# Optimization experiments

Measured on AMD Instinct MI355X. Metric: run time of the kernel, lower is better.

## Reference

```python
import jax, jax.numpy as jnp
import numpy as np

D_MODEL = 512
N_HEADS = 4  # d_model >= 8 -> 4 heads
HEAD_DIM = D_MODEL // N_HEADS
D_FF = 4 * D_MODEL


def setup_inputs() -> dict:
    key = jax.random.key(0)
    ks = jax.random.split(key, 8)
    B, T = 4, 2048
    s = 0.02
    return {
        "x": jax.random.normal(ks[0], (B, T, D_MODEL), dtype=jnp.float32),
        "ln1_g": jnp.ones((D_MODEL,), jnp.float32),
        "ln1_b": jnp.zeros((D_MODEL,), jnp.float32),
        "w_qkv": jax.random.normal(ks[1], (D_MODEL, 3 * D_MODEL), jnp.float32) * s,
        "w_proj": jax.random.normal(ks[2], (D_MODEL, D_MODEL), jnp.float32) * s,
        "ln2_g": jnp.ones((D_MODEL,), jnp.float32),
        "ln2_b": jnp.zeros((D_MODEL,), jnp.float32),
        "w_ff1": jax.random.normal(ks[3], (D_MODEL, D_FF), jnp.float32) * s,
        "w_ff2": jax.random.normal(ks[4], (D_FF, D_MODEL), jnp.float32) * s,
    }


def _layernorm(x, g, b, eps=1e-5):
    mu = jnp.mean(x, axis=-1, keepdims=True)
    var = jnp.var(x, axis=-1, keepdims=True)
    return (x - mu) * jax.lax.rsqrt(var + eps) * g + b


def _attention(x, w_qkv, w_proj):
    B, T, C = x.shape
    qkv = x @ w_qkv  # [B,T,3C]
    q, k, v = jnp.split(qkv, 3, axis=-1)
    # [B,H,T,Dh]
    q = q.reshape(B, T, N_HEADS, HEAD_DIM).transpose(0, 2, 1, 3)
    k = k.reshape(B, T, N_HEADS, HEAD_DIM).transpose(0, 2, 1, 3)
    v = v.reshape(B, T, N_HEADS, HEAD_DIM).transpose(0, 2, 1, 3)
    scale = 1.0 / jnp.sqrt(jnp.asarray(HEAD_DIM, x.dtype))
    scores = jnp.einsum("bhqd,bhkd->bhqk", q, k) * scale
    causal = jnp.tril(jnp.ones((T, T), bool))
    scores = jnp.where(causal, scores, -jnp.inf)
    attn = jax.nn.softmax(scores, axis=-1)
    out = jnp.einsum("bhqk,bhkd->bhqd", attn, v)
    out = out.transpose(0, 2, 1, 3).reshape(B, T, C)
    return out @ w_proj


def reference(x, ln1_g, ln1_b, w_qkv, w_proj, ln2_g, ln2_b, w_ff1, w_ff2):
    x = x + _attention(_layernorm(x, ln1_g, ln1_b), w_qkv, w_proj)
    h = _layernorm(x, ln2_g, ln2_b)
    h = jax.nn.gelu(h @ w_ff1, approximate=False) @ w_ff2
    return x + h
```

## Files before the change

### kernel.cpp

```cpp
#include <hip/hip_runtime.h>
#include <cstdint>

typedef unsigned short u16;
typedef __attribute__((ext_vector_type(8))) short short8;
typedef __attribute__((ext_vector_type(4))) float floatx4;

#define BT    8192
#define TSEQ  2048
#define NBAT  4
#define CMOD  512
#define NH    4
#define HD    128
#define DFF   2048
#define CQKV  1536

__device__ __forceinline__ u16 f2bf(float f) {
  union { float f; uint32_t u; } v; v.f = f;
  uint32_t r = v.u + 0x7FFFu + ((v.u >> 16) & 1u);
  return (u16)(r >> 16);
}
__device__ __forceinline__ float bf2f(u16 u) {
  union { uint32_t u; float f; } v; v.u = ((uint32_t)u) << 16; return v.f;
}
__device__ __forceinline__ float exp2a(float x) {
  float r; asm("v_exp_f32 %0, %1" : "=v"(r) : "v"(x)); return r;
}
__device__ __forceinline__ float rcpa(float x) {
  float r; asm("v_rcp_f32 %0, %1" : "=v"(r) : "v"(x)); return r;
}

typedef __attribute__((address_space(1))) const unsigned int ga_u32;
typedef __attribute__((address_space(3))) unsigned int ls_u32;
__device__ __forceinline__ void glds16(const u16* g, u16* l) {
  __builtin_amdgcn_global_load_lds((ga_u32*)g, (ls_u32*)l, 16, 0, 0);
}

__device__ __forceinline__ void tcast_body(const float* __restrict__ W, u16* __restrict__ Wt,
                                           int K, int N, int bx, int by, int tid,
                                           float (*tile)[33]) {
  int n0 = bx * 32, k0 = by * 32;
  int tx = tid & 31, ty = tid >> 5;
  #pragma unroll
  for (int r = 0; r < 32; r += 8)
    tile[r + ty][tx] = W[(size_t)(k0 + r + ty) * N + n0 + tx];
  __syncthreads();
  #pragma unroll
  for (int r = 0; r < 32; r += 8)
    Wt[(size_t)(n0 + r + ty) * K + k0 + tx] = f2bf(tile[tx][r + ty]);
}

__global__ __launch_bounds__(256) void prep_kernel(
    const float* __restrict__ x, const float* __restrict__ g, const float* __restrict__ b,
    const float* __restrict__ wqkv, const float* __restrict__ wproj,
    const float* __restrict__ wff1, const float* __restrict__ wff2,
    u16* __restrict__ ln_out, u16* __restrict__ wqkvT, u16* __restrict__ wprojT,
    u16* __restrict__ wff1T, u16* __restrict__ wff2T) {
  __shared__ float tile[32][33];
  int bid = blockIdx.x, tid = threadIdx.x;
  if (bid < 768) {
    tcast_body(wqkv, wqkvT, CMOD, CQKV, bid % 48, bid / 48, tid, tile);
  } else if (bid < 1024) {
    int id = bid - 768; tcast_body(wproj, wprojT, CMOD, CMOD, id % 16, id / 16, tid, tile);
  } else if (bid < 2048) {
    int id = bid - 1024; tcast_body(wff1, wff1T, CMOD, DFF, id % 64, id / 64, tid, tile);
  } else if (bid < 3072) {
    int id = bid - 2048; tcast_body(wff2, wff2T, DFF, CMOD, id % 16, id / 16, tid, tile);
  } else {
    int row = (bid - 3072) * 4 + (tid >> 6);
    int lane = tid & 63;
    const float4* xr = (const float4*)(x + (size_t)row * CMOD);
    float4 a = xr[lane], c = xr[lane + 64];
    float s = a.x + a.y + a.z + a.w + c.x + c.y + c.z + c.w;
    float q = a.x*a.x + a.y*a.y + a.z*a.z + a.w*a.w
            + c.x*c.x + c.y*c.y + c.z*c.z + c.w*c.w;
    #pragma unroll
    for (int o = 32; o; o >>= 1) { s += __shfl_xor(s, o); q += __shfl_xor(q, o); }
    float mu = s * (1.0f / CMOD);
    float rstd = rsqrtf(q * (1.0f / CMOD) - mu * mu + 1e-5f);
    const float4* gr = (const float4*)g;
    const float4* br = (const float4*)b;
    float4 g0 = gr[lane], g1 = gr[lane + 64], b0 = br[lane], b1 = br[lane + 64];
    u16* orow = ln_out + (size_t)row * CMOD;
    int i0 = lane * 4, i1 = (lane + 64) * 4;
    orow[i0 + 0] = f2bf((a.x - mu) * rstd * g0.x + b0.x);
    orow[i0 + 1] = f2bf((a.y - mu) * rstd * g0.y + b0.y);
    orow[i0 + 2] = f2bf((a.z - mu) * rstd * g0.z + b0.z);
    orow[i0 + 3] = f2bf((a.w - mu) * rstd * g0.w + b0.w);
    orow[i1 + 0] = f2bf((c.x - mu) * rstd * g1.x + b1.x);
    orow[i1 + 1] = f2bf((c.y - mu) * rstd * g1.y + b1.y);
    orow[i1 + 2] = f2bf((c.z - mu) * rstd * g1.z + b1.z);
    orow[i1 + 3] = f2bf((c.w - mu) * rstd * g1.w + b1.w);
  }
}

__global__ __launch_bounds__(256) void ln_kernel(const float* __restrict__ x,
                                                 const float* __restrict__ g,
                                                 const float* __restrict__ b,
                                                 u16* __restrict__ out) {
  int row = blockIdx.x * 4 + (threadIdx.x >> 6);
  int lane = threadIdx.x & 63;
  const float4* xr = (const float4*)(x + (size_t)row * CMOD);
  float4 a = xr[lane], c = xr[lane + 64];
  float s = a.x + a.y + a.z + a.w + c.x + c.y + c.z + c.w;
  float q = a.x*a.x + a.y*a.y + a.z*a.z + a.w*a.w
          + c.x*c.x + c.y*c.y + c.z*c.z + c.w*c.w;
  #pragma unroll
  for (int o = 32; o; o >>= 1) { s += __shfl_xor(s, o); q += __shfl_xor(q, o); }
  float mu = s * (1.0f / CMOD);
  float rstd = rsqrtf(q * (1.0f / CMOD) - mu * mu + 1e-5f);
  const float4* gr = (const float4*)g;
  const float4* br = (const float4*)b;
  float4 g0 = gr[lane], g1 = gr[lane + 64], b0 = br[lane], b1 = br[lane + 64];
  u16* orow = out + (size_t)row * CMOD;
  int i0 = lane * 4, i1 = (lane + 64) * 4;
  orow[i0 + 0] = f2bf((a.x - mu) * rstd * g0.x + b0.x);
  orow[i0 + 1] = f2bf((a.y - mu) * rstd * g0.y + b0.y);
  orow[i0 + 2] = f2bf((a.z - mu) * rstd * g0.z + b0.z);
  orow[i0 + 3] = f2bf((a.w - mu) * rstd * g0.w + b0.w);
  orow[i1 + 0] = f2bf((c.x - mu) * rstd * g1.x + b1.x);
  orow[i1 + 1] = f2bf((c.y - mu) * rstd * g1.y + b1.y);
  orow[i1 + 2] = f2bf((c.z - mu) * rstd * g1.z + b1.z);
  orow[i1 + 3] = f2bf((c.w - mu) * rstd * g1.w + b1.w);
}

template <int EPI, int TM, int TN, int MINW>
__global__ __launch_bounds__(256, MINW) void gemm_kernel(
    const u16* __restrict__ A, const u16* __restrict__ Bt, int K,
    const float* __restrict__ resid, float* __restrict__ outf,
    u16* __restrict__ ob0, u16* __restrict__ ob1, u16* __restrict__ ob2) {
  constexpr int MR  = TM / 32;
  constexpr int NR  = TN / 32;
  constexpr int NAR = TM / 64;
  constexpr int NBR = TN / 64;
  __shared__ __align__(16) u16 As[2][TM * 32];
  __shared__ __align__(16) u16 Bs[2][TN * 32];
  int tid = threadIdx.x;
  int lane = tid & 63, wave = tid >> 6;
  int lane16 = lane & 15, quad = lane >> 4;
  int m0 = blockIdx.y * TM, n0 = blockIdx.x * TN;
  int wm = (wave >> 1) * (TM / 2), wn = (wave & 1) * (TN / 2);

  floatx4 acc[MR][NR];
  #pragma unroll
  for (int i = 0; i < MR; i++)
    #pragma unroll
    for (int j = 0; j < NR; j++) acc[i][j] = (floatx4)(0.0f);

  const u16* agp[NAR]; u16* alp[NAR][2];
  const u16* bgp[NBR]; u16* blp[NBR][2];
  #pragma unroll
  for (int i = 0; i < NAR; i++) {
    int s = i * 256 + tid;
    agp[i] = A + (size_t)(m0 + (s >> 2)) * K + (s & 3) * 8;
    alp[i][0] = &As[0][(i * 256 + wave * 64) * 8];
    alp[i][1] = &As[1][(i * 256 + wave * 64) * 8];
  }
  #pragma unroll
  for (int i = 0; i < NBR; i++) {
    int s = i * 256 + tid;
    bgp[i] = Bt + (size_t)(n0 + (s >> 2)) * K + (s & 3) * 8;
    blp[i][0] = &Bs[0][(i * 256 + wave * 64) * 8];
    blp[i][1] = &Bs[1][(i * 256 + wave * 64) * 8];
  }

  int nk = K >> 5;
  #pragma unroll
  for (int i = 0; i < NAR; i++) glds16(agp[i], alp[i][0]);
  #pragma unroll
  for (int i = 0; i < NBR; i++) glds16(bgp[i], blp[i][0]);

  for (int kt = 0; kt < nk; kt++) {
    __syncthreads();
    int buf = kt & 1;
    if (kt + 1 < nk) {
      int k1 = (kt + 1) * 32;
      #pragma unroll
      for (int i = 0; i < NAR; i++) glds16(agp[i] + k1, alp[i][buf ^ 1]);
      #pragma unroll
      for (int i = 0; i < NBR; i++) glds16(bgp[i] + k1, blp[i][buf ^ 1]);
    }
    short8 af[MR];
    #pragma unroll
    for (int i = 0; i < MR; i++)
      af[i] = *(const short8*)&As[buf][(wm + i * 16 + lane16) * 32 + quad * 8];
    #pragma unroll
    for (int j = 0; j < NR; j++) {
      short8 bfj = *(const short8*)&Bs[buf][(wn + j * 16 + lane16) * 32 + quad * 8];
      #pragma unroll
      for (int i = 0; i < MR; i++)
        acc[i][j] = __builtin_amdgcn_mfma_f32_16x16x32_bf16(af[i], bfj, acc[i][j], 0, 0, 0);
    }
  }

  #pragma unroll
  for (int i = 0; i < MR; i++) {
    #pragma unroll
    for (int j = 0; j < NR; j++) {
      #pragma unroll
      for (int r = 0; r < 4; r++) {
        int m = m0 + wm + i * 16 + quad * 4 + r;
        int n = n0 + wn + j * 16 + lane16;
        float v = acc[i][j][r];
        if (EPI == 0) {
          int bb = m >> 11, t = m & 2047;
          int nn = n & 511, which = n >> 9;
          int h = nn >> 7, d = nn & 127;
          size_t base = (size_t)(bb * NH + h) * 262144;
          if (which == 0) {
            int t16 = t >> 4, l16 = t & 15, cc = d >> 5, qd = (d >> 3) & 3, e = d & 7;
            ob0[base + (size_t)((t16 * 16 + cc * 4 + qd) * 128 + l16 * 8 + e)] = f2bf(v * 0.12751743f);
          } else if (which == 1) {
            int kt = t >> 5, hf = (t >> 4) & 1, l16 = t & 15, cc = d >> 5, qd = (d >> 3) & 3, e = d & 7;
            ob1[base + (size_t)((kt * 8 + hf * 4 + cc) * 512 + qd * 128 + l16 * 8 + e)] = f2bf(v);
          } else {
            int kt = t >> 5, qv = (t >> 3) & 3, e = t & 7, j2 = d >> 4, l16 = d & 15;
            ob2[base + (size_t)((kt * 8 + j2) * 512 + qv * 128 + l16 * 8 + e)] = f2bf(v);
          }
        } else if (EPI == 1) {
          size_t idx = (size_t)m * CMOD + n;
          outf[idx] = v + resid[idx];
        } else if (EPI == 2) {
          float ge = 0.5f * v * (1.0f + erff(v * 0.70710678118654752f));
          ob0[(size_t)m * DFF + n] = f2bf(ge);
        } else {
          size_t idx = (size_t)m * CMOD + n;
          outf[idx] = v + resid[idx];
        }
      }
    }
  }
}

__global__ __launch_bounds__(256) void attn_kernel(const u16* __restrict__ qb,
                                                   const u16* __restrict__ kb,
                                                   const u16* __restrict__ vtb,
                                                   u16* __restrict__ po,
                                                   float* __restrict__ pl) {
  int tid = threadIdx.x, wave = tid >> 6, lane = tid & 63;
  int lane16 = lane & 15, quad = lane >> 4;
  int n1d = blockIdx.x;
  int bh = n1d & 15;
  int idx = 143 - (n1d >> 4);
  int g = 1;
  #pragma unroll
  for (int t = 2; t <= 8; t++) if (idx >= 2 * t * (t - 1)) g = t;
  int rem = idx - 2 * g * (g - 1);
  int qi = rem / g;
  int c  = rem - qi * g;
  int qt = ((g - 1) << 2) + qi;

  int q0w = qt * 64 + wave * 16;
  const u16* Qb = qb  + (size_t)bh * 262144;
  const u16* Kb = kb  + (size_t)bh * 262144;
  const u16* Vb = vtb + (size_t)bh * 262144;

  short8 aq[4];
  #pragma unroll
  for (int cc = 0; cc < 4; cc++)
    aq[cc] = *(const short8*)&Qb[(size_t)(((q0w >> 4) * 16 + cc * 4 + quad) * 128 + lane16 * 8)];

  int ktw   = (q0w >> 5) + 1;
  int ktblk = qt * 2 + 2;
  int kt0   = c * 8;
  int kend  = min(min(kt0 + 8, ktblk), ktw);

  floatx4 o[8];
  #pragma unroll
  for (int j = 0; j < 8; j++) o[j] = (floatx4)(0.0f);
  floatx4 ol = (floatx4)(0.0f);

  short8 ones;
  #pragma unroll
  for (int e = 0; e < 8; e++) ones[e] = (short)0x3F80;

  int addrA = (lane16 + ((quad & 1) << 5)) << 2;
  int addrB = addrA + 64;
  int q_g = q0w + lane16;

#define ATTN_TAIL(S0, S1, V_, KT)                                                                   \
  {                                                                                                 \
    int k0b = (KT) * 32 + quad * 4;                                                                 \
    _Pragma("unroll")                                                                               \
    for (int r = 0; r < 4; r++) {                                                                   \
      float p0 = exp2a(S0[r]);                                                                      \
      float p1 = exp2a(S1[r]);                                                                      \
      if (k0b + r > q_g) p0 = 0.0f;                                                                 \
      if (k0b + r + 16 > q_g) p1 = 0.0f;                                                            \
      S0[r] = p0; S1[r] = p1;                                                                       \
    }                                                                                               \
    uint32_t x0 = __builtin_amdgcn_perm(__float_as_uint(S0[1]), __float_as_uint(S0[0]), 0x07060302u); \
    uint32_t x1 = __builtin_amdgcn_perm(__float_as_uint(S0[3]), __float_as_uint(S0[2]), 0x07060302u); \
    uint32_t y0 = __builtin_amdgcn_perm(__float_as_uint(S1[1]), __float_as_uint(S1[0]), 0x07060302u); \
    uint32_t y1 = __builtin_amdgcn_perm(__float_as_uint(S1[3]), __float_as_uint(S1[2]), 0x07060302u); \
    int pAx0 = __builtin_amdgcn_ds_bpermute(addrA, (int)x0);                                        \
    int pAx1 = __builtin_amdgcn_ds_bpermute(addrA, (int)x1);                                        \
    int pBx0 = __builtin_amdgcn_ds_bpermute(addrB, (int)x0);                                        \
    int pBx1 = __builtin_amdgcn_ds_bpermute(addrB, (int)x1);                                        \
    int pAy0 = __builtin_amdgcn_ds_bpermute(addrA, (int)y0);                                        \
    int pAy1 = __builtin_amdgcn_ds_bpermute(addrA, (int)y1);                                        \
    int pBy0 = __builtin_amdgcn_ds_bpermute(addrB, (int)y0);                                        \
    int pBy1 = __builtin_amdgcn_ds_bpermute(addrB, (int)y1);                                        \
    union { uint32_t u[4]; short8 s; } pf;                                                          \
    bool hi = quad >= 2;                                                                            \
    pf.u[0] = (uint32_t)(hi ? pAy0 : pAx0);                                                         \
    pf.u[1] = (uint32_t)(hi ? pAy1 : pAx1);                                                         \
    pf.u[2] = (uint32_t)(hi ? pBy0 : pBx0);                                                         \
    pf.u[3] = (uint32_t)(hi ? pBy1 : pBx1);                                                         \
    _Pragma("unroll")                                                                               \
    for (int j = 0; j < 8; j++)                                                                     \
      o[j] = __builtin_amdgcn_mfma_f32_16x16x32_bf16(pf.s, V_[j], o[j], 0, 0, 0);                   \
    ol = __builtin_amdgcn_mfma_f32_16x16x32_bf16(pf.s, ones, ol, 0, 0, 0);                          \
  }

  int kt = kt0;
  for (; kt + 1 < kend; kt += 2) {
    const u16* kpa = Kb + (size_t)kt * 4096 + lane * 8;
    const u16* vpa = Vb + (size_t)kt * 4096 + lane * 8;
    short8 ka0[4], ka1[4], kb0[4], kb1[4], va[8], vb[8];
    #pragma unroll
    for (int cc = 0; cc < 4; cc++) {
      ka0[cc] = *(const short8*)&kpa[cc * 512];
      ka1[cc] = *(const short8*)&kpa[(4 + cc) * 512];
    }
    #pragma unroll
    for (int cc = 0; cc < 4; cc++) {
      kb0[cc] = *(const short8*)&kpa[4096 + cc * 512];
      kb1[cc] = *(const short8*)&kpa[4096 + (4 + cc) * 512];
    }
    #pragma unroll
    for (int j = 0; j < 8; j++) va[j] = *(const short8*)&vpa[j * 512];
    #pragma unroll
    for (int j = 0; j < 8; j++) vb[j] = *(const short8*)&vpa[4096 + j * 512];

    floatx4 sa0 = (floatx4)(0.0f), sa1 = (floatx4)(0.0f);
    #pragma unroll
    for (int cc = 0; cc < 4; cc++) {
      sa0 = __builtin_amdgcn_mfma_f32_16x16x32_bf16(ka0[cc], aq[cc], sa0, 0, 0, 0);
      sa1 = __builtin_amdgcn_mfma_f32_16x16x32_bf16(ka1[cc], aq[cc], sa1, 0, 0, 0);
    }
    floatx4 sb0 = (floatx4)(0.0f), sb1 = (floatx4)(0.0f);
    #pragma unroll
    for (int cc = 0; cc < 4; cc++) {
      sb0 = __builtin_amdgcn_mfma_f32_16x16x32_bf16(kb0[cc], aq[cc], sb0, 0, 0, 0);
      sb1 = __builtin_amdgcn_mfma_f32_16x16x32_bf16(kb1[cc], aq[cc], sb1, 0, 0, 0);
    }
    ATTN_TAIL(sa0, sa1, va, kt);
    ATTN_TAIL(sb0, sb1, vb, kt + 1);
  }
  if (kt < kend) {
    const u16* kp = Kb + (size_t)kt * 4096 + lane * 8;
    const u16* vp = Vb + (size_t)kt * 4096 + lane * 8;
    short8 k0f[4], k1f[4], vfr[8];
    #pragma unroll
    for (int cc = 0; cc < 4; cc++) {
      k0f[cc] = *(const short8*)&kp[cc * 512];
      k1f[cc] = *(const short8*)&kp[(4 + cc) * 512];
    }
    #pragma unroll
    for (int j = 0; j < 8; j++) vfr[j] = *(const short8*)&vp[j * 512];

    floatx4 st0 = (floatx4)(0.0f), st1 = (floatx4)(0.0f);
    #pragma unroll
    for (int cc = 0; cc < 4; cc++) {
      st0 = __builtin_amdgcn_mfma_f32_16x16x32_bf16(k0f[cc], aq[cc], st0, 0, 0, 0);
      st1 = __builtin_amdgcn_mfma_f32_16x16x32_bf16(k1f[cc], aq[cc], st1, 0, 0, 0);
    }
    ATTN_TAIL(st0, st1, vfr, kt);
  }
#undef ATTN_TAIL

  int slot = bh * 144 + 2 * g * (g - 1) + qi * g + c;
  u16* pob = po + (size_t)slot * 8192;
  #pragma unroll
  for (int r = 0; r < 4; r++) {
    int qr = wave * 16 + quad * 4 + r;
    #pragma unroll
    for (int j = 0; j < 8; j++)
      pob[qr * 128 + j * 16 + lane16] = f2bf(o[j][r]);
    if (lane16 == 0) pl[slot * 64 + qr] = ol[r];
  }
}

__global__ __launch_bounds__(256) void reduce_kernel(const u16* __restrict__ po,
                                                     const float* __restrict__ pl,
                                                     u16* __restrict__ attn) {
  int bh = blockIdx.x >> 5, qt = blockIdx.x & 31;
  int tid = threadIdx.x;
  int g = (qt >> 2) + 1;
  int slot0 = bh * 144 + 2 * g * (g - 1) + (qt & 3) * g;
  int qrow = tid >> 2;
  int d0 = (tid & 3) * 32;
  float acc[32];
  #pragma unroll
  for (int i = 0; i < 32; i++) acc[i] = 0.0f;
  float l = 0.0f;
  for (int c = 0; c < g; c++) {
    int slot = slot0 + c;
    l += pl[slot * 64 + qrow];
    const short8* p = (const short8*)(po + (size_t)slot * 8192 + qrow * 128 + d0);
    #pragma unroll
    for (int v = 0; v < 4; v++) {
      short8 pk = p[v];
      #pragma unroll
      for (int e = 0; e < 8; e++) acc[v * 8 + e] += bf2f((u16)pk[e]);
    }
  }
  float inv = rcpa(l);
  int b = bh >> 2, h = bh & 3, t = qt * 64 + qrow;
  u16* orow = attn + ((size_t)(b * TSEQ + t)) * CMOD + h * HD + d0;
  #pragma unroll
  for (int v = 0; v < 4; v++) {
    short8 ov;
    #pragma unroll
    for (int e = 0; e < 8; e++) ov[e] = (short)f2bf(acc[v * 8 + e] * inv);
    *(short8*)(orow + v * 8) = ov;
  }
}

extern "C" void kernel_launch(void* const* d_in, const int* in_sizes, int n_in,
                              void* d_out, int out_size, void* d_ws, size_t ws_size,
                              hipStream_t stream) {
  const float* x     = (const float*)d_in[0];
  const float* ln1g  = (const float*)d_in[1];
  const float* ln1b  = (const float*)d_in[2];
  const float* wqkv  = (const float*)d_in[3];
  const float* wproj = (const float*)d_in[4];
  const float* ln2g  = (const float*)d_in[5];
  const float* ln2b  = (const float*)d_in[6];
  const float* wff1  = (const float*)d_in[7];
  const float* wff2  = (const float*)d_in[8];
  float* out = (float*)d_out;
  char* ws = (char*)d_ws;

  u16* wt_qkv  = (u16*)(ws);
  u16* wt_proj = (u16*)(ws + 1572864);
  u16* wt_ff1  = (u16*)(ws + 2097152);
  u16* wt_ff2  = (u16*)(ws + 4194304);
  u16* ln_buf  = (u16*)(ws + 6291456);
  u16* q_buf   = (u16*)(ws + 14680064);
  u16* k_buf   = (u16*)(ws + 23068672);
  u16* vt_buf  = (u16*)(ws + 31457280);
  u16* attn    = (u16*)(ws + 39845888);
  float* x2    = (float*)(ws + 48234496);
  u16* h1      = (u16*)(ws + 65011712);
  u16* po      = (u16*)(ws + 48234496);
  float* pl    = (float*)(ws + 85983232);

  dim3 blk(256);
  prep_kernel<<<dim3(5120), blk, 0, stream>>>(x, ln1g, ln1b, wqkv, wproj, wff1, wff2,
                                              ln_buf, wt_qkv, wt_proj, wt_ff1, wt_ff2);

  gemm_kernel<0, 128, 64, 6><<<dim3(CQKV / 64, BT / 128), blk, 0, stream>>>(
      ln_buf, wt_qkv, CMOD, nullptr, nullptr, q_buf, k_buf, vt_buf);

  attn_kernel<<<dim3(2304), blk, 0, stream>>>(q_buf, k_buf, vt_buf, po, pl);

  reduce_kernel<<<dim3(512), blk, 0, stream>>>(po, pl, attn);

  gemm_kernel<1, 128, 64, 4><<<dim3(CMOD / 64, BT / 128), blk, 0, stream>>>(
      attn, wt_proj, CMOD, x, x2, nullptr, nullptr, nullptr);

  ln_kernel<<<dim3(BT / 4), blk, 0, stream>>>(x2, ln2g, ln2b, ln_buf);

  gemm_kernel<2, 128, 64, 6><<<dim3(DFF / 64, BT / 128), blk, 0, stream>>>(
      ln_buf, wt_ff1, CMOD, nullptr, nullptr, h1, nullptr, nullptr);

  gemm_kernel<3, 128, 64, 4><<<dim3(CMOD / 64, BT / 128), blk, 0, stream>>>(
      h1, wt_ff2, DFF, x2, out, nullptr, nullptr, nullptr);
}
```

Before: 269.9 us.

## Process two 16-row query tiles per wave to reuse K/V fragments

Each wave in the attention kernel now handles 32 query rows (two 16-row sub-tiles sharing the same K and V fragments) and the block shrinks to 128 threads. The goal is to halve global/L2 traffic for K and V per unit of MFMA work. The two-key-tile unroll is replaced by a single-tile loop that issues the V loads after the QK^T MFMAs. The cost is more live accumulator registers per wave, which may reduce occupancy. Masking and the key-tile bounds still hold because the wave's row range stays aligned to 32.

```diff
diff --git a/kernel.cpp b/kernel.cpp
--- a/kernel.cpp
+++ b/kernel.cpp
@@ -231,7 +231,7 @@
   }
 }
 
-__global__ __launch_bounds__(256) void attn_kernel(const u16* __restrict__ qb,
+__global__ __launch_bounds__(128) void attn_kernel(const u16* __restrict__ qb,
                                                    const u16* __restrict__ kb,
                                                    const u16* __restrict__ vtb,
                                                    u16* __restrict__ po,
@@ -249,25 +249,30 @@
   int c  = rem - qi * g;
   int qt = ((g - 1) << 2) + qi;
 
-  int q0w = qt * 64 + wave * 16;
+  int q0w = qt * 64 + wave * 32;
   const u16* Qb = qb  + (size_t)bh * 262144;
   const u16* Kb = kb  + (size_t)bh * 262144;
   const u16* Vb = vtb + (size_t)bh * 262144;
 
-  short8 aq[4];
-  #pragma unroll
-  for (int cc = 0; cc < 4; cc++)
-    aq[cc] = *(const short8*)&Qb[(size_t)(((q0w >> 4) * 16 + cc * 4 + quad) * 128 + lane16 * 8)];
+  short8 aqA[4], aqB[4];
+  {
+    int t16 = q0w >> 4;
+    #pragma unroll
+    for (int cc = 0; cc < 4; cc++) {
+      aqA[cc] = *(const short8*)&Qb[(size_t)((t16 * 16 + cc * 4 + quad) * 128 + lane16 * 8)];
+      aqB[cc] = *(const short8*)&Qb[(size_t)(((t16 + 1) * 16 + cc * 4 + quad) * 128 + lane16 * 8)];
+    }
+  }
 
   int ktw   = (q0w >> 5) + 1;
   int ktblk = qt * 2 + 2;
   int kt0   = c * 8;
   int kend  = min(min(kt0 + 8, ktblk), ktw);
 
-  floatx4 o[8];
-  #pragma unroll
-  for (int j = 0; j < 8; j++) o[j] = (floatx4)(0.0f);
-  floatx4 ol = (floatx4)(0.0f);
+  floatx4 oA[8], oB[8];
+  #pragma unroll
+  for (int j = 0; j < 8; j++) { oA[j] = (floatx4)(0.0f); oB[j] = (floatx4)(0.0f); }
+  floatx4 olA = (floatx4)(0.0f), olB = (floatx4)(0.0f);
 
   short8 ones;
   #pragma unroll
@@ -275,17 +280,18 @@
 
   int addrA = (lane16 + ((quad & 1) << 5)) << 2;
   int addrB = addrA + 64;
-  int q_g = q0w + lane16;
-
-#define ATTN_TAIL(S0, S1, V_, KT)                                                                   \
+  int q_gA = q0w + lane16;
+  int q_gB = q0w + 16 + lane16;
+
+#define ATTN_TAIL(S0, S1, O_, OL_, QG, KT)                                                          \
   {                                                                                                 \
     int k0b = (KT) * 32 + quad * 4;                                                                 \
     _Pragma("unroll")                                                                               \
     for (int r = 0; r < 4; r++) {                                                                   \
       float p0 = exp2a(S0[r]);                                                                      \
       float p1 = exp2a(S1[r]);                                                                      \
-      if (k0b + r > q_g) p0 = 0.0f;                                                                 \
-      if (k0b + r + 16 > q_g) p1 = 0.0f;                                                            \
+      if (k0b + r > (QG)) p0 = 0.0f;                                                                \
+      if (k0b + r + 16 > (QG)) p1 = 0.0f;                                                           \
       S0[r] = p0; S1[r] = p1;                                                                       \
     }                                                                                               \
     uint32_t x0 = __builtin_amdgcn_perm(__float_as_uint(S0[1]), __float_as_uint(S0[0]), 0x07060302u); \
@@ -308,64 +314,37 @@
     pf.u[3] = (uint32_t)(hi ? pBy1 : pBx1);                                                         \
     _Pragma("unroll")                                                                               \
     for (int j = 0; j < 8; j++)                                                                     \
-      o[j] = __builtin_amdgcn_mfma_f32_16x16x32_bf16(pf.s, V_[j], o[j], 0, 0, 0);                   \
-    ol = __builtin_amdgcn_mfma_f32_16x16x32_bf16(pf.s, ones, ol, 0, 0, 0);                          \
-  }
-
-  int kt = kt0;
-  for (; kt + 1 < kend; kt += 2) {
-    const u16* kpa = Kb + (size_t)kt * 4096 + lane * 8;
-    const u16* vpa = Vb + (size_t)kt * 4096 + lane * 8;
-    short8 ka0[4], ka1[4], kb0[4], kb1[4], va[8], vb[8];
-    #pragma unroll
-    for (int cc = 0; cc < 4; cc++) {
-      ka0[cc] = *(const short8*)&kpa[cc * 512];
-      ka1[cc] = *(const short8*)&kpa[(4 + cc) * 512];
-    }
-    #pragma unroll
-    for (int cc = 0; cc < 4; cc++) {
-      kb0[cc] = *(const short8*)&kpa[4096 + cc * 512];
-      kb1[cc] = *(const short8*)&kpa[4096 + (4 + cc) * 512];
-    }
-    #pragma unroll
-    for (int j = 0; j < 8; j++) va[j] = *(const short8*)&vpa[j * 512];
-    #pragma unroll
-    for (int j = 0; j < 8; j++) vb[j] = *(const short8*)&vpa[4096 + j * 512];
-
-    floatx4 sa0 = (floatx4)(0.0f), sa1 = (floatx4)(0.0f);
-    #pragma unroll
-    for (int cc = 0; cc < 4; cc++) {
-      sa0 = __builtin_amdgcn_mfma_f32_16x16x32_bf16(ka0[cc], aq[cc], sa0, 0, 0, 0);
-      sa1 = __builtin_amdgcn_mfma_f32_16x16x32_bf16(ka1[cc], aq[cc], sa1, 0, 0, 0);
-    }
-    floatx4 sb0 = (floatx4)(0.0f), sb1 = (floatx4)(0.0f);
-    #pragma unroll
-    for (int cc = 0; cc < 4; cc++) {
-      sb0 = __builtin_amdgcn_mfma_f32_16x16x32_bf16(kb0[cc], aq[cc], sb0, 0, 0, 0);
-      sb1 = __builtin_amdgcn_mfma_f32_16x16x32_bf16(kb1[cc], aq[cc], sb1, 0, 0, 0);
-    }
-    ATTN_TAIL(sa0, sa1, va, kt);
-    ATTN_TAIL(sb0, sb1, vb, kt + 1);
-  }
-  if (kt < kend) {
+      O_[j] = __builtin_amdgcn_mfma_f32_16x16x32_bf16(pf.s, vfr[j], O_[j], 0, 0, 0);                \
+    OL_ = __builtin_amdgcn_mfma_f32_16x16x32_bf16(pf.s, ones, OL_, 0, 0, 0);                        \
+  }
+
+  for (int kt = kt0; kt < kend; kt++) {
     const u16* kp = Kb + (size_t)kt * 4096 + lane * 8;
     const u16* vp = Vb + (size_t)kt * 4096 + lane * 8;
-    short8 k0f[4], k1f[4], vfr[8];
+    short8 k0f[4], k1f[4];
     #pragma unroll
     for (int cc = 0; cc < 4; cc++) {
       k0f[cc] = *(const short8*)&kp[cc * 512];
       k1f[cc] = *(const short8*)&kp[(4 + cc) * 512];
     }
-    #pragma unroll
-    for (int j = 0; j < 8; j++) vfr[j] = *(const short8*)&vp[j * 512];
-
-    floatx4 st0 = (floatx4)(0.0f), st1 = (floatx4)(0.0f);
+
+    floatx4 sA0 = (floatx4)(0.0f), sA1 = (floatx4)(0.0f);
+    floatx4 sB0 = (floatx4)(0.0f), sB1 = (floatx4)(0.0f);
     #pragma unroll
     for (int cc = 0; cc < 4; cc++) {
-      st0 = __builtin_amdgcn_mfma_f32_16x16x32_bf16(k0f[cc], aq[cc], st0, 0, 0, 0);
-      st1 = __builtin_amdgcn_mfma_f32_16x16x32_bf16(k1f[cc], aq[cc], st1, 0, 0, 0);
-    }
-    ATTN_TAIL(st0, st1, vfr, kt);
+      sA0 = __builtin_amdgcn_mfma_f32_16x16x32_bf16(k0f[cc], aqA[cc], sA0, 0, 0, 0);
+      sA1 = __builtin_amdgcn_mfma_f32_16x16x32_bf16(k1f[cc], aqA[cc], sA1, 0, 0, 0);
+      sB0 = __builtin_amdgcn_mfma_f32_16x16x32_bf16(k0f[cc], aqB[cc], sB0, 0, 0, 0);
+      sB1 = __builtin_amdgcn_mfma_f32_16x16x32_bf16(k1f[cc], aqB[cc], sB1, 0, 0, 0);
+    }
+
+    short8 vfr[8];
+    #pragma unroll
+    for (int j = 0; j < 8; j++)
+      vfr[j] = *(const short8*)&vp[j * 512];
+
+    ATTN_TAIL(sA0, sA1, oA, olA, q_gA, kt);
+    ATTN_TAIL(sB0, sB1, oB, olB, q_gB, kt);
   }
 #undef ATTN_TAIL
 
@@ -373,11 +352,17 @@
   u16* pob = po + (size_t)slot * 8192;
   #pragma unroll
   for (int r = 0; r < 4; r++) {
-    int qr = wave * 16 + quad * 4 + r;
-    #pragma unroll
-    for (int j = 0; j < 8; j++)
-      pob[qr * 128 + j * 16 + lane16] = f2bf(o[j][r]);
-    if (lane16 == 0) pl[slot * 64 + qr] = ol[r];
+    int qrA = wave * 32 + quad * 4 + r;
+    int qrB = qrA + 16;
+    #pragma unroll
+    for (int j = 0; j < 8; j++) {
+      pob[qrA * 128 + j * 16 + lane16] = f2bf(oA[j][r]);
+      pob[qrB * 128 + j * 16 + lane16] = f2bf(oB[j][r]);
+    }
+    if (lane16 == 0) {
+      pl[slot * 64 + qrA] = olA[r];
+      pl[slot * 64 + qrB] = olB[r];
+    }
   }
 }
 
@@ -453,7 +438,7 @@
   gemm_kernel<0, 128, 64, 6><<<dim3(CQKV / 64, BT / 128), blk, 0, stream>>>(
       ln_buf, wt_qkv, CMOD, nullptr, nullptr, q_buf, k_buf, vt_buf);
 
-  attn_kernel<<<dim3(2304), blk, 0, stream>>>(q_buf, k_buf, vt_buf, po, pl);
+  attn_kernel<<<dim3(2304), dim3(128), 0, stream>>>(q_buf, k_buf, vt_buf, po, pl);
 
   reduce_kernel<<<dim3(512), blk, 0, stream>>>(po, pl, attn);
 
```

New measurement: 265.0 us. About the same (-1.8%).
